# Performance work log

Hardware: AMD Instinct MI355X
Metric: run time of the kernel (lower is better)

## Reference

```python
import jax, jax.numpy as jnp
import numpy as np
import math

EMBED = 768
N_HEAD = 12
HEAD = EMBED // N_HEAD
RADIUS = 128
POS_SIZE = 2 * RADIUS
B, S = 8, 1024


def setup_inputs() -> dict:
    key = jax.random.key(0)
    ks = jax.random.split(key, 6)
    x = jax.random.normal(ks[0], (B, S, EMBED), dtype=jnp.float32)
    # torch Linear weights have shape [out, in]; y = x @ W.T
    Wq = jax.random.normal(ks[1], (EMBED, EMBED), dtype=jnp.float32) * 0.02
    Wk = jax.random.normal(ks[2], (EMBED, EMBED), dtype=jnp.float32) * 0.02
    Wv = jax.random.normal(ks[3], (EMBED, EMBED), dtype=jnp.float32) * 0.02
    Wp = jax.random.normal(ks[4], (EMBED, EMBED), dtype=jnp.float32) * 0.02
    pos_emb_k = jax.random.normal(ks[5], (POS_SIZE, HEAD), dtype=jnp.float32) * 0.02
    return {"x": x, "Wq": Wq, "Wk": Wk, "Wv": Wv, "Wp": Wp, "pos_emb_k": pos_emb_k}


def reference(x, Wq, Wk, Wv, Wp, pos_emb_k):
    b, s, e = x.shape
    # projections -> [B, H, S, D]
    def split_heads(t):
        return t.reshape(b, s, N_HEAD, HEAD).transpose(0, 2, 1, 3)
    q = split_heads(x @ Wq.T)
    k = split_heads(x @ Wk.T)
    v = split_heads(x @ Wv.T)
    # relative-position logits: [B, H, S, 2R]
    att_rel_pos = jnp.einsum('bhsd,pd->bhsp', q, pos_emb_k)
    # index map: clamp(j - i, -R, R-1) mod 2R -> [S, S]
    rel = jnp.arange(s)[None, :] - jnp.arange(s)[:, None]
    att_idxs = jnp.clip(rel, -RADIUS, RADIUS - 1) % POS_SIZE
    idxs = jnp.broadcast_to(att_idxs[None, None], (b, N_HEAD, s, s))
    att_pos = jnp.take_along_axis(att_rel_pos, idxs, axis=3)  # [B, H, S, S]
    att_val = jnp.einsum('bhqd,bhkd->bhqk', q, k)
    att = jax.nn.softmax((att_val + att_pos) * (1.0 / math.sqrt(HEAD)), axis=-1)
    y = jnp.einsum('bhqk,bhkd->bhqd', att, v)
    y = y.transpose(0, 2, 1, 3).reshape(b, s, e)
    return y @ Wp.T
```

## Files before the change

### kernel.cpp

```cpp
#include <hip/hip_runtime.h>

#define NB 8
#define NS 1024
#define NE 768
#define NH 12
#define ND 64

typedef __attribute__((ext_vector_type(8))) short bf16x8;
typedef __attribute__((ext_vector_type(4))) float f32x4;
typedef __attribute__((ext_vector_type(16))) float f32x16;
typedef const __attribute__((address_space(1))) void gv_t;
typedef __attribute__((address_space(3))) void sv_t;

static __device__ __forceinline__ ushort f2bf(float f) {
  union { float f; unsigned u; } c; c.f = f;
  unsigned u = c.u + 0x7fffu + ((c.u >> 16) & 1u);
  return (ushort)(u >> 16);
}
static __device__ __forceinline__ float bf2f(ushort h) {
  union { unsigned u; float f; } c; c.u = ((unsigned)h) << 16;
  return c.f;
}
static __device__ __forceinline__ uint pk_bf16(float lo, float hi) {
  uint r;
  asm("v_cvt_pk_bf16_f32 %0, %1, %2" : "=v"(r) : "v"(lo), "v"(hi));
  return r;
}
#define PL32SWAP(a, b) asm("v_permlane32_swap_b32 %0, %1" : "+v"(a), "+v"(b))
#define GLDS16(src, dst) __builtin_amdgcn_global_load_lds((gv_t*)(src), (sv_t*)(dst), 16, 0, 0)

__global__ void cvt_x(const float* __restrict__ src, ushort* __restrict__ dst) {
  int i = (blockIdx.x * 256 + threadIdx.x) * 4;
  float4 f = *(const float4*)(src + i);
  ushort4 o;
  o.x = f2bf(f.x); o.y = f2bf(f.y); o.z = f2bf(f.z); o.w = f2bf(f.w);
  *(ushort4*)(dst + i) = o;
}

__global__ void cvt_weights(const float* __restrict__ w0, const float* __restrict__ w1,
                            const float* __restrict__ w2, const float* __restrict__ w3,
                            const float* __restrict__ w4,
                            ushort* __restrict__ o0, ushort* __restrict__ o1,
                            ushort* __restrict__ o2, ushort* __restrict__ o3,
                            ushort* __restrict__ o4) {
  int blk = blockIdx.x;
  const float* src; ushort* dst; int idx;
  if (blk < 2304) {
    int ws = blk / 576, b = blk % 576;
    src = (ws == 0) ? w0 : (ws == 1) ? w1 : (ws == 2) ? w2 : w3;
    dst = (ws == 0) ? o0 : (ws == 1) ? o1 : (ws == 2) ? o2 : o3;
    idx = b;
  } else {
    src = w4; dst = o4; idx = blk - 2304;
  }
  int i = (idx * 256 + threadIdx.x) * 4;
  float4 f = *(const float4*)(src + i);
  ushort4 o;
  o.x = f2bf(f.x); o.y = f2bf(f.y); o.z = f2bf(f.z); o.w = f2bf(f.w);
  *(ushort4*)(dst + i) = o;
}

__device__ __forceinline__ void gemm_core(const ushort* __restrict__ A,
                                          const ushort* __restrict__ Bw,
                                          ushort* As, ushort* Bs,
                                          int bm0, int bn0, f32x4 (&acc)[4][4]) {
  const int tid = threadIdx.x;
  const int w = tid >> 6, lane = tid & 63;
  const int l15 = lane & 15, l4 = lane >> 4;
  const int wm = w >> 1, wn = w & 1;
  const int row = tid >> 2, seg = tid & 3;

  #pragma unroll 1
  for (int kt = 0; kt < 24; ++kt) {
    __syncthreads();
    #pragma unroll
    for (int p = 0; p < 2; ++p) {
      const ushort* ga = A + (size_t)(bm0 + p * 64 + row) * 768 + kt * 32 + seg * 8;
      GLDS16(ga, As + (p * 256 + w * 64) * 8);
      const ushort* gb = Bw + (size_t)(bn0 + p * 64 + row) * 768 + kt * 32 + seg * 8;
      GLDS16(gb, Bs + (p * 256 + w * 64) * 8);
    }
    __syncthreads();

    bf16x8 af[4], bf[4];
    #pragma unroll
    for (int mi = 0; mi < 4; ++mi)
      af[mi] = *(const bf16x8*)(As + (wm * 64 + mi * 16 + l15) * 32 + l4 * 8);
    #pragma unroll
    for (int ni = 0; ni < 4; ++ni)
      bf[ni] = *(const bf16x8*)(Bs + (wn * 64 + ni * 16 + l15) * 32 + l4 * 8);
    #pragma unroll
    for (int mi = 0; mi < 4; ++mi)
      #pragma unroll
      for (int ni = 0; ni < 4; ++ni)
        acc[mi][ni] = __builtin_amdgcn_mfma_f32_16x16x32_bf16(af[mi], bf[ni], acc[mi][ni], 0, 0, 0);
  }
}

__global__ __launch_bounds__(256)
void gemm_qkv(const ushort* __restrict__ A,
              const ushort* __restrict__ B0, const ushort* __restrict__ B1, const ushort* __restrict__ B2,
              ushort* __restrict__ C0, ushort* __restrict__ C1, ushort* __restrict__ C2) {
  __shared__ __align__(16) char gsm[34816];
  ushort* As = (ushort*)gsm;
  ushort* Bs = As + 4096;
  ushort* VtS = (ushort*)gsm;

  const int wsel = blockIdx.y / 6;
  const int bn0 = (blockIdx.y % 6) * 128;
  const int bm0 = blockIdx.x * 128;
  const ushort* Bw = (wsel == 0) ? B0 : (wsel == 1) ? B1 : B2;
  ushort* Co = (wsel == 0) ? C0 : (wsel == 1) ? C1 : C2;

  f32x4 acc[4][4];
  #pragma unroll
  for (int i = 0; i < 4; ++i)
    #pragma unroll
    for (int j = 0; j < 4; ++j)
      acc[i][j] = (f32x4){0.f, 0.f, 0.f, 0.f};

  gemm_core(A, Bw, As, Bs, bm0, bn0, acc);

  const int tid = threadIdx.x;
  const int lane = tid & 63;
  const int w = tid >> 6;
  const int l15 = lane & 15, l4 = lane >> 4;
  const int wm = w >> 1, wn = w & 1;

  if (wsel == 2) {
    __syncthreads();
    #pragma unroll
    for (int mi = 0; mi < 4; ++mi) {
      #pragma unroll
      for (int ni = 0; ni < 4; ++ni) {
        const int nl = wn * 64 + ni * 16 + l15;
        const int ml = wm * 64 + mi * 16 + l4 * 4;
        ushort4 pk;
        pk.x = f2bf(acc[mi][ni][0]); pk.y = f2bf(acc[mi][ni][1]);
        pk.z = f2bf(acc[mi][ni][2]); pk.w = f2bf(acc[mi][ni][3]);
        *(ushort4*)&VtS[nl * 136 + ml] = pk;
      }
    }
    __syncthreads();
    #pragma unroll
    for (int p = 0; p < 8; ++p) {
      const int n = p * 16 + (tid >> 4);
      const int m = (tid & 15) * 8;
      bf16x8 vv = *(const bf16x8*)&VtS[n * 136 + m];
      const int ng = bn0 + n, h = ng >> 6, d = ng & 63;
      const int mg = bm0 + m, b = mg >> 10, sl = mg & 1023;
      size_t off = (size_t)(b * NH + h) * 65536 + (size_t)(sl >> 5) * 2048
                 + (d & 31) * 64 + (d >> 5) * 32 + (sl & 31);
      *(bf16x8*)&Co[off] = vv;
    }
  } else {
    const float scl = (wsel == 0) ? 0.18033688f : 1.0f;
    #pragma unroll
    for (int mi = 0; mi < 4; ++mi) {
      #pragma unroll
      for (int ni = 0; ni < 4; ++ni) {
        #pragma unroll
        for (int e = 0; e < 4; ++e) {
          int m = bm0 + wm * 64 + mi * 16 + l4 * 4 + e;
          int n = bn0 + wn * 64 + ni * 16 + l15;
          int b = m >> 10, s = m & 1023, h = n >> 6, d = n & 63;
          Co[(size_t)(b * NH + h) * 65536 + (s << 6) + d] = f2bf(acc[mi][ni][e] * scl);
        }
      }
    }
  }
}

__global__ __launch_bounds__(256)
void gemm_proj(const ushort* __restrict__ A, const ushort* __restrict__ Bw,
               float* __restrict__ Cout) {
  __shared__ ushort As[128 * 32];
  __shared__ ushort Bs[128 * 32];
  const int bm0 = blockIdx.x * 128;
  const int bn0 = blockIdx.y * 128;

  f32x4 acc[4][4];
  #pragma unroll
  for (int i = 0; i < 4; ++i)
    #pragma unroll
    for (int j = 0; j < 4; ++j)
      acc[i][j] = (f32x4){0.f, 0.f, 0.f, 0.f};

  gemm_core(A, Bw, As, Bs, bm0, bn0, acc);

  const int lane = threadIdx.x & 63;
  const int w = threadIdx.x >> 6;
  const int l15 = lane & 15, l4 = lane >> 4;
  const int wm = w >> 1, wn = w & 1;
  #pragma unroll
  for (int mi = 0; mi < 4; ++mi) {
    #pragma unroll
    for (int ni = 0; ni < 4; ++ni) {
      #pragma unroll
      for (int e = 0; e < 4; ++e) {
        int m = bm0 + wm * 64 + mi * 16 + l4 * 4 + e;
        int n = bn0 + wn * 64 + ni * 16 + l15;
        Cout[(size_t)m * NE + n] = acc[mi][ni][e];
      }
    }
  }
}

#define FINISH_CHUNK(S, VF00, VF01, VF10, VF11)                               \
  {                                                                           \
    float m01 = fmaxf(S[0], S[1]),  m23 = fmaxf(S[2], S[3]);                  \
    float m45 = fmaxf(S[4], S[5]),  m67 = fmaxf(S[6], S[7]);                  \
    float m89 = fmaxf(S[8], S[9]),  mab = fmaxf(S[10], S[11]);                \
    float mcd = fmaxf(S[12], S[13]), mef = fmaxf(S[14], S[15]);               \
    float cmax = fmaxf(fmaxf(fmaxf(m01, m23), fmaxf(m45, m67)),               \
                       fmaxf(fmaxf(m89, mab), fmaxf(mcd, mef)));              \
    cmax = fmaxf(cmax, __shfl_xor(cmax, 32));                                 \
    const float m_new = fmaxf(m_run, cmax);                                   \
    if (__any(m_new - m_run > 8.f)) {                                         \
      const float sc = __builtin_amdgcn_exp2f(m_run - m_new);                 \
      l_run *= sc;                                                            \
      m_run = m_new;                                                          \
      _Pragma("unroll")                                                       \
      for (int i = 0; i < 16; ++i) { o0[i] *= sc; o1[i] *= sc; }              \
    }                                                                         \
    float ls = 0.f;                                                           \
    _Pragma("unroll")                                                         \
    for (int i = 0; i < 16; ++i) {                                            \
      S[i] = __builtin_amdgcn_exp2f(S[i] - m_run);                            \
      ls += S[i];                                                             \
    }                                                                         \
    l_run += ls;                                                              \
    uint a0 = pk_bf16(S[0],  S[1]);                                           \
    uint a1 = pk_bf16(S[2],  S[3]);                                           \
    uint a2 = pk_bf16(S[4],  S[5]);                                           \
    uint a3 = pk_bf16(S[6],  S[7]);                                           \
    uint a4 = pk_bf16(S[8],  S[9]);                                           \
    uint a5 = pk_bf16(S[10], S[11]);                                          \
    uint a6 = pk_bf16(S[12], S[13]);                                          \
    uint a7 = pk_bf16(S[14], S[15]);                                          \
    PL32SWAP(a0, a2);                                                         \
    PL32SWAP(a1, a3);                                                         \
    PL32SWAP(a4, a6);                                                         \
    PL32SWAP(a5, a7);                                                         \
    union FU { bf16x8 v; uint u[4]; } f0, f1;                                 \
    f0.u[0] = a0; f0.u[1] = a1; f0.u[2] = a2; f0.u[3] = a3;                   \
    f1.u[0] = a4; f1.u[1] = a5; f1.u[2] = a6; f1.u[3] = a7;                   \
    __builtin_amdgcn_s_setprio(1);                                            \
    o0 = __builtin_amdgcn_mfma_f32_32x32x16_bf16(VF00, f0.v, o0, 0, 0, 0);    \
    o0 = __builtin_amdgcn_mfma_f32_32x32x16_bf16(VF01, f1.v, o0, 0, 0, 0);    \
    o1 = __builtin_amdgcn_mfma_f32_32x32x16_bf16(VF10, f0.v, o1, 0, 0, 0);    \
    o1 = __builtin_amdgcn_mfma_f32_32x32x16_bf16(VF11, f1.v, o1, 0, 0, 0);    \
    __builtin_amdgcn_s_setprio(0);                                            \
  }

static __device__ __forceinline__ f32x16 bias_init(int dlt, const ushort* RlRow,
                                                   float c_lo, float c_hi,
                                                   int half4, int il) {
  f32x16 s;
  if (dlt <= -160 || dlt >= 160) {
    const float cv = (dlt < 0) ? c_lo : c_hi;
    #pragma unroll
    for (int i = 0; i < 16; ++i) s[i] = cv;
  } else {
    #pragma unroll
    for (int i = 0; i < 16; ++i) {
      const int rr = (i & 3) + 8 * (i >> 2) + half4;
      int rel = dlt + rr - il;
      rel = rel < -128 ? -128 : (rel > 127 ? 127 : rel);
      s[i] = bf2f(RlRow[rel & 255]);
    }
  }
  return s;
}

__global__ __launch_bounds__(256, 3)
void attn_kernel(const ushort* __restrict__ q, const ushort* __restrict__ k,
                 const ushort* __restrict__ vt3, const ushort* __restrict__ pe,
                 ushort* __restrict__ y) {
  __shared__ __align__(16) char smem[50688];
  ushort* Rl = (ushort*)smem;
  float* OL  = (float*)smem;
  float* ML  = (float*)(smem + 16896);
  ushort* Ks = (ushort*)(smem + 17920);
  ushort* Vs = (ushort*)(smem + 34304);

  const int tid = threadIdx.x;
  const int w = tid >> 6, lane = tid & 63;
  const int il = lane & 31;
  const int hb = lane >> 5;
  const int hi8 = hb * 8;
  const int half4 = hb * 4;

  const int bid = blockIdx.x;
  const int swz_b = (bid & 7) * 384 + (bid >> 3);
  const int bh = swz_b >> 5;
  const int q0 = (swz_b & 31) * 32;

  const ushort* qp = q + (size_t)bh * 65536;
  const ushort* kp = k + (size_t)bh * 65536;
  const ushort* vp = vt3 + (size_t)bh * 65536;

  const int laneoff = ((lane >> 3) << 6) + (((lane & 7) ^ ((lane >> 3) & 7)) << 3);
  const ushort* kpre = kp + laneoff + w * 16384;
  const ushort* vpre = vp + laneoff + w * 16384;
  ushort* KsW = Ks + w * 2048;
  ushort* VsW = Vs + w * 2048;
  const int fswz = (il & 7) << 3;
  const ushort* Kr = KsW + il * 64;
  const ushort* Vr = VsW + il * 64;

  bf16x8 qf[4];
  #pragma unroll
  for (int ks = 0; ks < 4; ++ks)
    qf[ks] = *(const bf16x8*)(qp + (q0 + il) * 64 + ks * 16 + hi8);

  #pragma unroll
  for (int t = 0; t < 4; ++t) {
    GLDS16(kpre + t * 512, KsW + t * 512);
    GLDS16(vpre + t * 512, VsW + t * 512);
  }

  #pragma unroll
  for (int pb = 0; pb < 2; ++pb) {
    const int pc0 = (w * 2 + pb) * 32;
    f32x16 r;
    #pragma unroll
    for (int i = 0; i < 16; ++i) r[i] = 0.f;
    #pragma unroll
    for (int ks = 0; ks < 4; ++ks) {
      bf16x8 pf = *(const bf16x8*)(pe + (pc0 + il) * 64 + ks * 16 + hi8);
      r = __builtin_amdgcn_mfma_f32_32x32x16_bf16(qf[ks], pf, r, 0, 0, 0);
    }
    #pragma unroll
    for (int i = 0; i < 16; ++i) {
      const int rr = (i & 3) + 8 * (i >> 2) + half4;
      Rl[rr * 258 + pc0 + il] = f2bf(r[i]);
    }
  }
  __syncthreads();

  const ushort* RlRow = Rl + il * 258;
  const float c_lo = bf2f(RlRow[128]);
  const float c_hi = bf2f(RlRow[127]);

  float m_run = -1e30f, l_run = 0.f;
  f32x16 o0, o1;
  #pragma unroll
  for (int i = 0; i < 16; ++i) { o0[i] = 0.f; o1[i] = 0.f; }

  f32x16 s_pipe = bias_init(w * 256 - q0, RlRow, c_lo, c_hi, half4, il);
  asm volatile("s_waitcnt vmcnt(0)" ::: "memory");
  __builtin_amdgcn_sched_barrier(0);
  bf16x8 kf0 = *(const bf16x8*)(Kr + ((0 * 16 + hi8) ^ fswz));
  bf16x8 kf1 = *(const bf16x8*)(Kr + ((1 * 16 + hi8) ^ fswz));
  bf16x8 kf2 = *(const bf16x8*)(Kr + ((2 * 16 + hi8) ^ fswz));
  bf16x8 kf3 = *(const bf16x8*)(Kr + ((3 * 16 + hi8) ^ fswz));
  bf16x8 vfp0 = *(const bf16x8*)(Vr + ((hi8) ^ fswz));
  bf16x8 vfp1 = *(const bf16x8*)(Vr + ((16 + hi8) ^ fswz));
  bf16x8 vfp2 = *(const bf16x8*)(Vr + ((32 + hi8) ^ fswz));
  bf16x8 vfp3 = *(const bf16x8*)(Vr + ((48 + hi8) ^ fswz));
  asm volatile("s_waitcnt lgkmcnt(0)" ::: "memory");
  __builtin_amdgcn_sched_barrier(0);
  #pragma unroll
  for (int t = 0; t < 4; ++t) {
    GLDS16(kpre + 2048 + t * 512, KsW + t * 512);
    GLDS16(vpre + 2048 + t * 512, VsW + t * 512);
  }
  __builtin_amdgcn_s_setprio(1);
  s_pipe = __builtin_amdgcn_mfma_f32_32x32x16_bf16(kf0, qf[0], s_pipe, 0, 0, 0);
  s_pipe = __builtin_amdgcn_mfma_f32_32x32x16_bf16(kf1, qf[1], s_pipe, 0, 0, 0);
  s_pipe = __builtin_amdgcn_mfma_f32_32x32x16_bf16(kf2, qf[2], s_pipe, 0, 0, 0);
  s_pipe = __builtin_amdgcn_mfma_f32_32x32x16_bf16(kf3, qf[3], s_pipe, 0, 0, 0);
  __builtin_amdgcn_s_setprio(0);

  #pragma unroll 1
  for (int c = 0; c < 7; ++c) {
    f32x16 s2 = bias_init(w * 256 + (c + 1) * 32 - q0, RlRow, c_lo, c_hi, half4, il);
    asm volatile("s_waitcnt vmcnt(0)" ::: "memory");
    __builtin_amdgcn_sched_barrier(0);
    kf0 = *(const bf16x8*)(Kr + ((0 * 16 + hi8) ^ fswz));
    kf1 = *(const bf16x8*)(Kr + ((1 * 16 + hi8) ^ fswz));
    kf2 = *(const bf16x8*)(Kr + ((2 * 16 + hi8) ^ fswz));
    kf3 = *(const bf16x8*)(Kr + ((3 * 16 + hi8) ^ fswz));
    bf16x8 vfn0 = *(const bf16x8*)(Vr + ((hi8) ^ fswz));
    bf16x8 vfn1 = *(const bf16x8*)(Vr + ((16 + hi8) ^ fswz));
    bf16x8 vfn2 = *(const bf16x8*)(Vr + ((32 + hi8) ^ fswz));
    bf16x8 vfn3 = *(const bf16x8*)(Vr + ((48 + hi8) ^ fswz));
    asm volatile("s_waitcnt lgkmcnt(0)" ::: "memory");
    __builtin_amdgcn_sched_barrier(0);
    if (c < 6) {
      const ushort* kn = kpre + (c + 2) * 2048;
      const ushort* vn = vpre + (c + 2) * 2048;
      #pragma unroll
      for (int t = 0; t < 4; ++t) {
        GLDS16(kn + t * 512, KsW + t * 512);
        GLDS16(vn + t * 512, VsW + t * 512);
      }
    }
    __builtin_amdgcn_s_setprio(1);
    s2 = __builtin_amdgcn_mfma_f32_32x32x16_bf16(kf0, qf[0], s2, 0, 0, 0);
    s2 = __builtin_amdgcn_mfma_f32_32x32x16_bf16(kf1, qf[1], s2, 0, 0, 0);
    s2 = __builtin_amdgcn_mfma_f32_32x32x16_bf16(kf2, qf[2], s2, 0, 0, 0);
    s2 = __builtin_amdgcn_mfma_f32_32x32x16_bf16(kf3, qf[3], s2, 0, 0, 0);
    __builtin_amdgcn_s_setprio(0);

    FINISH_CHUNK(s_pipe, vfp0, vfp1, vfp2, vfp3);

    s_pipe = s2;
    vfp0 = vfn0; vfp1 = vfn1; vfp2 = vfn2; vfp3 = vfn3;
  }

  FINISH_CHUNK(s_pipe, vfp0, vfp1, vfp2, vfp3);

  l_run += __shfl_xor(l_run, 32);

  __syncthreads();
  #pragma unroll
  for (int i = 0; i < 16; ++i) {
    const int rr = (i & 3) + 8 * (i >> 2) + half4;
    OL[(w * 32 + rr) * 33 + il] = o0[i];
  }
  if (hb == 0) {
    ML[(w * 2) * 32 + il] = m_run;
    ML[(w * 2 + 1) * 32 + il] = l_run;
  }
  __syncthreads();

  const int mq = tid >> 3;
  const int dg = (tid & 7) * 4;
  float mw[4], lw[4];
  #pragma unroll
  for (int wv = 0; wv < 4; ++wv) {
    mw[wv] = ML[(wv * 2) * 32 + mq];
    lw[wv] = ML[(wv * 2 + 1) * 32 + mq];
  }
  const float ms = fmaxf(fmaxf(mw[0], mw[1]), fmaxf(mw[2], mw[3]));
  float cw[4], lst = 0.f;
  #pragma unroll
  for (int wv = 0; wv < 4; ++wv) {
    cw[wv] = __builtin_amdgcn_exp2f(mw[wv] - ms);
    lst += cw[wv] * lw[wv];
  }
  const float inv = 1.f / lst;

  float r0[4] = {0.f, 0.f, 0.f, 0.f};
  #pragma unroll
  for (int wv = 0; wv < 4; ++wv)
    #pragma unroll
    for (int e = 0; e < 4; ++e)
      r0[e] += cw[wv] * OL[(wv * 32 + dg + e) * 33 + mq];

  __syncthreads();
  #pragma unroll
  for (int i = 0; i < 16; ++i) {
    const int rr = (i & 3) + 8 * (i >> 2) + half4;
    OL[(w * 32 + rr) * 33 + il] = o1[i];
  }
  __syncthreads();

  float r1[4] = {0.f, 0.f, 0.f, 0.f};
  #pragma unroll
  for (int wv = 0; wv < 4; ++wv)
    #pragma unroll
    for (int e = 0; e < 4; ++e)
      r1[e] += cw[wv] * OL[(wv * 32 + dg + e) * 33 + mq];

  const int b = bh / NH, h = bh % NH;
  ushort* yrow = y + (size_t)(b * NS + q0 + mq) * NE + h * 64;
  ushort4 s0, s1;
  s0.x = f2bf(r0[0] * inv); s0.y = f2bf(r0[1] * inv);
  s0.z = f2bf(r0[2] * inv); s0.w = f2bf(r0[3] * inv);
  s1.x = f2bf(r1[0] * inv); s1.y = f2bf(r1[1] * inv);
  s1.z = f2bf(r1[2] * inv); s1.w = f2bf(r1[3] * inv);
  *(ushort4*)(yrow + dg) = s0;
  *(ushort4*)(yrow + 32 + dg) = s1;
}

extern "C" void kernel_launch(void* const* d_in, const int* in_sizes, int n_in,
                              void* d_out, int out_size, void* d_ws, size_t ws_size,
                              hipStream_t stream) {
  const float* x  = (const float*)d_in[0];
  const float* Wq = (const float*)d_in[1];
  const float* Wk = (const float*)d_in[2];
  const float* Wv = (const float*)d_in[3];
  const float* Wp = (const float*)d_in[4];
  const float* pe = (const float*)d_in[5];

  ushort* ws  = (ushort*)d_ws;
  ushort* xb  = ws;
  ushort* wqb = xb  + 6291456;
  ushort* wkb = wqb + 589824;
  ushort* wvb = wkb + 589824;
  ushort* wpb = wvb + 589824;
  ushort* peb = wpb + 589824;
  ushort* qb  = peb + 16384;
  ushort* kb  = qb  + 6291456;
  ushort* vtb = kb  + 6291456;
  ushort* yb  = vtb + 6291456;

  cvt_x<<<dim3(6144), dim3(256), 0, stream>>>(x, xb);
  cvt_weights<<<dim3(2320), dim3(256), 0, stream>>>(Wq, Wk, Wv, Wp, pe,
                                                    wqb, wkb, wvb, wpb, peb);
  gemm_qkv<<<dim3(64, 18), dim3(256), 0, stream>>>(xb, wqb, wkb, wvb, qb, kb, vtb);
  attn_kernel<<<dim3(3072), dim3(256), 0, stream>>>(qb, kb, vtb, peb, yb);
  gemm_proj<<<dim3(64, 6), dim3(256), 0, stream>>>(yb, wpb, (float*)d_out);
}
```

Before: 163.0 us.

## Store K/V in MFMA-fragment layout and load directly to registers

The QKV GEMM now writes K and V^T in a per-chunk layout that matches the MFMA operand fragments, so each lane can read its 16-byte fragment straight from global memory with one coalesced load. The attention kernel drops the LDS staging for K and V, along with the vmcnt/lgkmcnt waits, and double-buffers fragments in registers across a fully unrolled 8-chunk loop. LDS use falls from about 50 KB to about 18 KB per block, which may raise occupancy, but register pressure grows and global-load latency is now hidden only by register prefetch two chunks ahead.

```diff
diff --git a/kernel.cpp b/kernel.cpp
--- a/kernel.cpp
+++ b/kernel.cpp
@@ -150,11 +150,29 @@
       const int ng = bn0 + n, h = ng >> 6, d = ng & 63;
       const int mg = bm0 + m, b = mg >> 10, sl = mg & 1023;
       size_t off = (size_t)(b * NH + h) * 65536 + (size_t)(sl >> 5) * 2048
-                 + (d & 31) * 64 + (d >> 5) * 32 + (sl & 31);
+                 + (size_t)((d >> 5) * 2 + ((sl >> 4) & 1)) * 512
+                 + ((sl >> 3) & 1) * 256 + (d & 31) * 8;
       *(bf16x8*)&Co[off] = vv;
     }
+  } else if (wsel == 1) {
+    #pragma unroll
+    for (int mi = 0; mi < 4; ++mi) {
+      #pragma unroll
+      for (int ni = 0; ni < 4; ++ni) {
+        #pragma unroll
+        for (int e = 0; e < 4; ++e) {
+          int m = bm0 + wm * 64 + mi * 16 + l4 * 4 + e;
+          int n = bn0 + wn * 64 + ni * 16 + l15;
+          int b = m >> 10, s = m & 1023, h = n >> 6, d = n & 63;
+          size_t off = (size_t)(b * NH + h) * 65536 + (size_t)(s >> 5) * 2048
+                     + (size_t)(d >> 4) * 512 + ((d >> 3) & 1) * 256
+                     + (s & 31) * 8 + (d & 7);
+          Co[off] = f2bf(acc[mi][ni][e]);
+        }
+      }
+    }
   } else {
-    const float scl = (wsel == 0) ? 0.18033688f : 1.0f;
+    const float scl = 0.18033688f;
     #pragma unroll
     for (int mi = 0; mi < 4; ++mi) {
       #pragma unroll
@@ -273,16 +291,39 @@
   return s;
 }
 
+#define LOADK(P, C)                                                           \
+  k##P##0 = *(const bf16x8*)(kc + (C) * 2048);                                \
+  k##P##1 = *(const bf16x8*)(kc + (C) * 2048 + 512);                          \
+  k##P##2 = *(const bf16x8*)(kc + (C) * 2048 + 1024);                         \
+  k##P##3 = *(const bf16x8*)(kc + (C) * 2048 + 1536);
+#define LOADV(P, C)                                                           \
+  v##P##0 = *(const bf16x8*)(vc + (C) * 2048);                                \
+  v##P##1 = *(const bf16x8*)(vc + (C) * 2048 + 512);                          \
+  v##P##2 = *(const bf16x8*)(vc + (C) * 2048 + 1024);                         \
+  v##P##3 = *(const bf16x8*)(vc + (C) * 2048 + 1536);
+
+#define CHUNK(C, P)                                                           \
+  {                                                                           \
+    f32x16 s = bias_init(w * 256 + (C) * 32 - q0, RlRow, c_lo, c_hi, half4, il); \
+    __builtin_amdgcn_s_setprio(1);                                            \
+    s = __builtin_amdgcn_mfma_f32_32x32x16_bf16(k##P##0, qf[0], s, 0, 0, 0);  \
+    s = __builtin_amdgcn_mfma_f32_32x32x16_bf16(k##P##1, qf[1], s, 0, 0, 0);  \
+    s = __builtin_amdgcn_mfma_f32_32x32x16_bf16(k##P##2, qf[2], s, 0, 0, 0);  \
+    s = __builtin_amdgcn_mfma_f32_32x32x16_bf16(k##P##3, qf[3], s, 0, 0, 0);  \
+    __builtin_amdgcn_s_setprio(0);                                            \
+    if ((C) + 2 < 8) { LOADK(P, (C) + 2) }                                    \
+    FINISH_CHUNK(s, v##P##0, v##P##1, v##P##2, v##P##3);                      \
+    if ((C) + 2 < 8) { LOADV(P, (C) + 2) }                                    \
+  }
+
 __global__ __launch_bounds__(256, 3)
-void attn_kernel(const ushort* __restrict__ q, const ushort* __restrict__ k,
-                 const ushort* __restrict__ vt3, const ushort* __restrict__ pe,
+void attn_kernel(const ushort* __restrict__ q, const ushort* __restrict__ k4,
+                 const ushort* __restrict__ v4, const ushort* __restrict__ pe,
                  ushort* __restrict__ y) {
-  __shared__ __align__(16) char smem[50688];
+  __shared__ __align__(16) char smem[17920];
   ushort* Rl = (ushort*)smem;
   float* OL  = (float*)smem;
   float* ML  = (float*)(smem + 16896);
-  ushort* Ks = (ushort*)(smem + 17920);
-  ushort* Vs = (ushort*)(smem + 34304);
 
   const int tid = threadIdx.x;
   const int w = tid >> 6, lane = tid & 63;
@@ -297,28 +338,18 @@
   const int q0 = (swz_b & 31) * 32;
 
   const ushort* qp = q + (size_t)bh * 65536;
-  const ushort* kp = k + (size_t)bh * 65536;
-  const ushort* vp = vt3 + (size_t)bh * 65536;
-
-  const int laneoff = ((lane >> 3) << 6) + (((lane & 7) ^ ((lane >> 3) & 7)) << 3);
-  const ushort* kpre = kp + laneoff + w * 16384;
-  const ushort* vpre = vp + laneoff + w * 16384;
-  ushort* KsW = Ks + w * 2048;
-  ushort* VsW = Vs + w * 2048;
-  const int fswz = (il & 7) << 3;
-  const ushort* Kr = KsW + il * 64;
-  const ushort* Vr = VsW + il * 64;
+  const ushort* kc = k4 + (size_t)bh * 65536 + w * 16384 + lane * 8;
+  const ushort* vc = v4 + (size_t)bh * 65536 + w * 16384 + lane * 8;
 
   bf16x8 qf[4];
   #pragma unroll
   for (int ks = 0; ks < 4; ++ks)
     qf[ks] = *(const bf16x8*)(qp + (q0 + il) * 64 + ks * 16 + hi8);
 
-  #pragma unroll
-  for (int t = 0; t < 4; ++t) {
-    GLDS16(kpre + t * 512, KsW + t * 512);
-    GLDS16(vpre + t * 512, VsW + t * 512);
-  }
+  bf16x8 ka0, ka1, ka2, ka3, va0, va1, va2, va3;
+  bf16x8 kb0, kb1, kb2, kb3, vb0, vb1, vb2, vb3;
+  LOADK(a, 0) LOADV(a, 0)
+  LOADK(b, 1) LOADV(b, 1)
 
   #pragma unroll
   for (int pb = 0; pb < 2; ++pb) {
@@ -348,69 +379,14 @@
   #pragma unroll
   for (int i = 0; i < 16; ++i) { o0[i] = 0.f; o1[i] = 0.f; }
 
-  f32x16 s_pipe = bias_init(w * 256 - q0, RlRow, c_lo, c_hi, half4, il);
-  asm volatile("s_waitcnt vmcnt(0)" ::: "memory");
-  __builtin_amdgcn_sched_barrier(0);
-  bf16x8 kf0 = *(const bf16x8*)(Kr + ((0 * 16 + hi8) ^ fswz));
-  bf16x8 kf1 = *(const bf16x8*)(Kr + ((1 * 16 + hi8) ^ fswz));
-  bf16x8 kf2 = *(const bf16x8*)(Kr + ((2 * 16 + hi8) ^ fswz));
-  bf16x8 kf3 = *(const bf16x8*)(Kr + ((3 * 16 + hi8) ^ fswz));
-  bf16x8 vfp0 = *(const bf16x8*)(Vr + ((hi8) ^ fswz));
-  bf16x8 vfp1 = *(const bf16x8*)(Vr + ((16 + hi8) ^ fswz));
-  bf16x8 vfp2 = *(const bf16x8*)(Vr + ((32 + hi8) ^ fswz));
-  bf16x8 vfp3 = *(const bf16x8*)(Vr + ((48 + hi8) ^ fswz));
-  asm volatile("s_waitcnt lgkmcnt(0)" ::: "memory");
-  __builtin_amdgcn_sched_barrier(0);
-  #pragma unroll
-  for (int t = 0; t < 4; ++t) {
-    GLDS16(kpre + 2048 + t * 512, KsW + t * 512);
-    GLDS16(vpre + 2048 + t * 512, VsW + t * 512);
-  }
-  __builtin_amdgcn_s_setprio(1);
-  s_pipe = __builtin_amdgcn_mfma_f32_32x32x16_bf16(kf0, qf[0], s_pipe, 0, 0, 0);
-  s_pipe = __builtin_amdgcn_mfma_f32_32x32x16_bf16(kf1, qf[1], s_pipe, 0, 0, 0);
-  s_pipe = __builtin_amdgcn_mfma_f32_32x32x16_bf16(kf2, qf[2], s_pipe, 0, 0, 0);
-  s_pipe = __builtin_amdgcn_mfma_f32_32x32x16_bf16(kf3, qf[3], s_pipe, 0, 0, 0);
-  __builtin_amdgcn_s_setprio(0);
-
-  #pragma unroll 1
-  for (int c = 0; c < 7; ++c) {
-    f32x16 s2 = bias_init(w * 256 + (c + 1) * 32 - q0, RlRow, c_lo, c_hi, half4, il);
-    asm volatile("s_waitcnt vmcnt(0)" ::: "memory");
-    __builtin_amdgcn_sched_barrier(0);
-    kf0 = *(const bf16x8*)(Kr + ((0 * 16 + hi8) ^ fswz));
-    kf1 = *(const bf16x8*)(Kr + ((1 * 16 + hi8) ^ fswz));
-    kf2 = *(const bf16x8*)(Kr + ((2 * 16 + hi8) ^ fswz));
-    kf3 = *(const bf16x8*)(Kr + ((3 * 16 + hi8) ^ fswz));
-    bf16x8 vfn0 = *(const bf16x8*)(Vr + ((hi8) ^ fswz));
-    bf16x8 vfn1 = *(const bf16x8*)(Vr + ((16 + hi8) ^ fswz));
-    bf16x8 vfn2 = *(const bf16x8*)(Vr + ((32 + hi8) ^ fswz));
-    bf16x8 vfn3 = *(const bf16x8*)(Vr + ((48 + hi8) ^ fswz));
-    asm volatile("s_waitcnt lgkmcnt(0)" ::: "memory");
-    __builtin_amdgcn_sched_barrier(0);
-    if (c < 6) {
-      const ushort* kn = kpre + (c + 2) * 2048;
-      const ushort* vn = vpre + (c + 2) * 2048;
-      #pragma unroll
-      for (int t = 0; t < 4; ++t) {
-        GLDS16(kn + t * 512, KsW + t * 512);
-        GLDS16(vn + t * 512, VsW + t * 512);
-      }
-    }
-    __builtin_amdgcn_s_setprio(1);
-    s2 = __builtin_amdgcn_mfma_f32_32x32x16_bf16(kf0, qf[0], s2, 0, 0, 0);
-    s2 = __builtin_amdgcn_mfma_f32_32x32x16_bf16(kf1, qf[1], s2, 0, 0, 0);
-    s2 = __builtin_amdgcn_mfma_f32_32x32x16_bf16(kf2, qf[2], s2, 0, 0, 0);
-    s2 = __builtin_amdgcn_mfma_f32_32x32x16_bf16(kf3, qf[3], s2, 0, 0, 0);
-    __builtin_amdgcn_s_setprio(0);
-
-    FINISH_CHUNK(s_pipe, vfp0, vfp1, vfp2, vfp3);
-
-    s_pipe = s2;
-    vfp0 = vfn0; vfp1 = vfn1; vfp2 = vfn2; vfp3 = vfn3;
-  }
-
-  FINISH_CHUNK(s_pipe, vfp0, vfp1, vfp2, vfp3);
+  CHUNK(0, a)
+  CHUNK(1, b)
+  CHUNK(2, a)
+  CHUNK(3, b)
+  CHUNK(4, a)
+  CHUNK(5, b)
+  CHUNK(6, a)
+  CHUNK(7, b)
 
   l_run += __shfl_xor(l_run, 32);
 
@@ -494,14 +470,14 @@
   ushort* wpb = wvb + 589824;
   ushort* peb = wpb + 589824;
   ushort* qb  = peb + 16384;
-  ushort* kb  = qb  + 6291456;
-  ushort* vtb = kb  + 6291456;
-  ushort* yb  = vtb + 6291456;
+  ushort* k4b = qb  + 6291456;
+  ushort* v4b = k4b + 6291456;
+  ushort* yb  = v4b + 6291456;
 
   cvt_x<<<dim3(6144), dim3(256), 0, stream>>>(x, xb);
   cvt_weights<<<dim3(2320), dim3(256), 0, stream>>>(Wq, Wk, Wv, Wp, pe,
                                                     wqb, wkb, wvb, wpb, peb);
-  gemm_qkv<<<dim3(64, 18), dim3(256), 0, stream>>>(xb, wqb, wkb, wvb, qb, kb, vtb);
-  attn_kernel<<<dim3(3072), dim3(256), 0, stream>>>(qb, kb, vtb, peb, yb);
+  gemm_qkv<<<dim3(64, 18), dim3(256), 0, stream>>>(xb, wqb, wkb, wvb, qb, k4b, v4b);
+  attn_kernel<<<dim3(3072), dim3(256), 0, stream>>>(qb, k4b, v4b, peb, yb);
   gemm_proj<<<dim3(64, 6), dim3(256), 0, stream>>>(yb, wpb, (float*)d_out);
 }
```

Result: faster. 154.4 us (-5.3%).
